# Optimization experiments

Measured on AMD Instinct MI355X. Metric: run time of the kernel, lower is better.

The kernel has to match this reference:

```python
import jax, jax.numpy as jnp
import numpy as np

E, F, NF = 16, 128, 64          # elevators, per-elevator feature size, num_floors
PRE, CI, CH, OUT = 64, 64, 32, 128
R, DROPOFF = 3, 0.333


def _cell(x, h, c, Wih, Whh, bih, bhh, alpha=1.0):
    # torch LSTM cell; alpha scales the candidate-state update (alpha-LSTM).
    g = x @ Wih.T + bih + h @ Whh.T + bhh
    i, f, gg, o = jnp.split(g, 4, axis=-1)
    c2 = jax.nn.sigmoid(f) * c + alpha * jax.nn.sigmoid(i) * jnp.tanh(gg)
    h2 = jax.nn.sigmoid(o) * jnp.tanh(c2)
    return h2, c2


def _forward(features, pre_h, pre_c, out_h, out_c,
             pre_Wih0, pre_Whh0, pre_bih0, pre_bhh0,
             pre_Wih1, pre_Whh1, pre_bih1, pre_bhh1,
             fc_W, fc_b,
             comm_Wih0, comm_Whh0, comm_bih0, comm_bhh0,
             comm_Wih1, comm_Whh1, comm_bih1, comm_bhh1,
             out_Wih, out_Whh, out_bih, out_bhh,
             tar_W, tar_b, dir_W, dir_b):
    # alpha schedule: round r uses dropoff**r, same alpha for all E elevators in a round
    alphas = jnp.repeat(jnp.float32(DROPOFF) ** jnp.arange(R, dtype=jnp.float32), E)

    def step(carry, feat_t):
        ph, pc, oh, oc = carry                       # [E,2,PRE] x2, [E,OUT] x2
        feat = feat_t.reshape(E, F)
        # 2-layer preprocess LSTM, seq len 1, vectorized over elevators
        h0, c0 = _cell(feat, ph[:, 0], pc[:, 0], pre_Wih0, pre_Whh0, pre_bih0, pre_bhh0)
        h1, c1 = _cell(h0,   ph[:, 1], pc[:, 1], pre_Wih1, pre_Whh1, pre_bih1, pre_bhh1)
        x = jax.nn.leaky_relu(h1 @ fc_W.T + fc_b, 0.05)   # [E, CI]
        # sequential communication: rounds x elevators through shared alpha-LSTM state
        xs = jnp.tile(x, (R, 1))                          # [R*E, CI]
        z = jnp.zeros((CH,), feat.dtype)

        def comm_step(cst, xi_a):
            ch0, cc0, ch1, cc1 = cst
            xi, a = xi_a
            nh0, nc0 = _cell(xi, ch0, cc0, comm_Wih0, comm_Whh0, comm_bih0, comm_bhh0, a)
            nh1, nc1 = _cell(nh0, ch1, cc1, comm_Wih1, comm_Whh1, comm_bih1, comm_bhh1, a)
            return (nh0, nc0, nh1, nc1), None

        (ch0, cc0, ch1, cc1), _ = jax.lax.scan(comm_step, (z, z, z, z), (xs, alphas))
        group = jnp.concatenate([cc0, cc1])               # comm cell state flattened [2*CH]
        # postprocessing LSTM (1 layer) + heads, per elevator
        out_in = jnp.concatenate([jnp.broadcast_to(group, (E, 2 * CH)), feat], axis=1)
        noh, noc = _cell(out_in, oh, oc, out_Wih, out_Whh, out_bih, out_bhh)
        tar = jax.nn.softmax(noh @ tar_W.T + tar_b, axis=-1)
        dire = jax.nn.softmax(noh @ dir_W.T + dir_b, axis=-1)
        out = jnp.concatenate([tar, dire], axis=1)        # [E, NF+3]
        new_carry = (jnp.stack([h0, h1], 1), jnp.stack([c0, c1], 1), noh, noc)
        return new_carry, out

    _, outs = jax.lax.scan(step, (pre_h, pre_c, out_h, out_c), features)
    return outs  # [B, E, NF+3]


def setup_inputs() -> dict:
    key = jax.random.key(0)
    ks = iter(jax.random.split(key, 40))

    def p(shape, fan):
        return jax.random.uniform(next(ks), shape, jnp.float32, -1.0, 1.0) / np.sqrt(fan)

    B = 2048
    return {
        "features": jax.random.normal(next(ks), (B, E * F), jnp.float32),
        "pre_h": jnp.zeros((E, 2, PRE), jnp.float32),
        "pre_c": jnp.zeros((E, 2, PRE), jnp.float32),
        "out_h": jnp.zeros((E, OUT), jnp.float32),
        "out_c": jnp.zeros((E, OUT), jnp.float32),
        "pre_Wih0": p((4 * PRE, F), PRE), "pre_Whh0": p((4 * PRE, PRE), PRE),
        "pre_bih0": p((4 * PRE,), PRE), "pre_bhh0": p((4 * PRE,), PRE),
        "pre_Wih1": p((4 * PRE, PRE), PRE), "pre_Whh1": p((4 * PRE, PRE), PRE),
        "pre_bih1": p((4 * PRE,), PRE), "pre_bhh1": p((4 * PRE,), PRE),
        "fc_W": p((CI, PRE), PRE), "fc_b": p((CI,), PRE),
        "comm_Wih0": p((4 * CH, CI), CH), "comm_Whh0": p((4 * CH, CH), CH),
        "comm_bih0": p((4 * CH,), CH), "comm_bhh0": p((4 * CH,), CH),
        "comm_Wih1": p((4 * CH, CH), CH), "comm_Whh1": p((4 * CH, CH), CH),
        "comm_bih1": p((4 * CH,), CH), "comm_bhh1": p((4 * CH,), CH),
        "out_Wih": p((4 * OUT, F + 2 * CH), OUT), "out_Whh": p((4 * OUT, OUT), OUT),
        "out_bih": p((4 * OUT,), OUT), "out_bhh": p((4 * OUT,), OUT),
        "tar_W": p((NF, OUT), OUT), "tar_b": p((NF,), OUT),
        "dir_W": p((3, OUT), OUT), "dir_b": p((3,), OUT),
    }


def reference(features, pre_h, pre_c, out_h, out_c,
              pre_Wih0, pre_Whh0, pre_bih0, pre_bhh0,
              pre_Wih1, pre_Whh1, pre_bih1, pre_bhh1,
              fc_W, fc_b,
              comm_Wih0, comm_Whh0, comm_bih0, comm_bhh0,
              comm_Wih1, comm_Whh1, comm_bih1, comm_bhh1,
              out_Wih, out_Whh, out_bih, out_bhh,
              tar_W, tar_b, dir_W, dir_b):
    return _forward(features, pre_h, pre_c, out_h, out_c,
                    pre_Wih0, pre_Whh0, pre_bih0, pre_bhh0,
                    pre_Wih1, pre_Whh1, pre_bih1, pre_bhh1,
                    fc_W, fc_b,
                    comm_Wih0, comm_Whh0, comm_bih0, comm_bhh0,
                    comm_Wih1, comm_Whh1, comm_bih1, comm_bhh1,
                    out_Wih, out_Whh, out_bih, out_bhh,
                    tar_W, tar_b, dir_W, dir_b)
```

## Files before the change

kernel.cpp:

```cpp
#include <hip/hip_runtime.h>
#include <hip/hip_bf16.h>


#define E_ 16
#define F_ 128

typedef int i4 __attribute__((ext_vector_type(4)));
typedef _Float16 hf;
typedef hf hf2 __attribute__((ext_vector_type(2)));

__device__ __forceinline__ float sigf(float x) { return 1.0f / (1.0f + __expf(-x)); }
__device__ __forceinline__ float tanhf_(float x) {
  float e = __expf(2.0f * x);
  return 1.0f - 2.0f / (e + 1.0f);
}
__device__ __forceinline__ float lane_bcast(float v, int k) {
  return __int_as_float(__builtin_amdgcn_readlane(__float_as_int(v), k));
}
__device__ __forceinline__ float fdot2(int a, int b, float c) {
#if __has_builtin(__builtin_amdgcn_fdot2)
  return __builtin_amdgcn_fdot2(__builtin_bit_cast(hf2, a),
                                __builtin_bit_cast(hf2, b), c, false);
#else
  float d;
  asm("v_dot2_f32_f16 %0, %1, %2, %3" : "=v"(d) : "v"(a), "v"(b), "v"(c));
  return d;
#endif
}

__device__ __forceinline__ float dpp_xor1(float x) {
  return __int_as_float(__builtin_amdgcn_update_dpp(
      __float_as_int(x), __float_as_int(x), 0xB1, 0xF, 0xF, true));
}
__device__ __forceinline__ float dpp_xor2(float x) {
  return __int_as_float(__builtin_amdgcn_update_dpp(
      __float_as_int(x), __float_as_int(x), 0x4E, 0xF, 0xF, true));
}

__global__ void f2h_kernel(const float* __restrict__ src, hf* __restrict__ dst, int n) {
  int i = blockIdx.x * 256 + threadIdx.x;
  if (i < n) dst[i] = (hf)src[i];
}

__global__ __launch_bounds__(256) void gemm_k(
    const float* __restrict__ A, int lda,
    const float* __restrict__ W, int ldw, int co,
    const float* __restrict__ b1, const float* __restrict__ b2,
    float* __restrict__ C, int N, int K) {
  __shared__ float As[64 * 65];
  __shared__ float Ws[128 * 65];
  const int tid = threadIdx.x;
  const int m0 = blockIdx.x * 64;
  const int n0 = blockIdx.y * 128;
  const int rr = tid >> 4;
  const int c4 = (tid & 15) << 2;
  const int tm = tid >> 4;
  const int tn = tid & 15;

  float acc[4][8];
#pragma unroll
  for (int i = 0; i < 4; ++i)
#pragma unroll
    for (int j = 0; j < 8; ++j) acc[i][j] = 0.0f;

  for (int kk = 0; kk < K; kk += 64) {
#pragma unroll
    for (int p = 0; p < 4; ++p) {
      const int r = rr + p * 16;
      const float4 v = *(const float4*)(A + (size_t)(m0 + r) * lda + kk + c4);
      float* dst = &As[r * 65 + c4];
      dst[0] = v.x; dst[1] = v.y; dst[2] = v.z; dst[3] = v.w;
    }
#pragma unroll
    for (int p = 0; p < 8; ++p) {
      const int n = rr + p * 16;
      const float4 v = *(const float4*)(W + (size_t)(n0 + n) * ldw + co + kk + c4);
      float* dst = &Ws[n * 65 + c4];
      dst[0] = v.x; dst[1] = v.y; dst[2] = v.z; dst[3] = v.w;
    }
    __syncthreads();
#pragma unroll 4
    for (int k = 0; k < 64; ++k) {
      float a[4], wv[8];
#pragma unroll
      for (int i = 0; i < 4; ++i) a[i] = As[(tm * 4 + i) * 65 + k];
#pragma unroll
      for (int j = 0; j < 8; ++j) wv[j] = Ws[(tn * 8 + j) * 65 + k];
#pragma unroll
      for (int i = 0; i < 4; ++i)
#pragma unroll
        for (int j = 0; j < 8; ++j) acc[i][j] += a[i] * wv[j];
    }
    __syncthreads();
  }
#pragma unroll
  for (int i = 0; i < 4; ++i) {
    const int m = m0 + tm * 4 + i;
#pragma unroll
    for (int j = 0; j < 8; ++j) {
      const int n = n0 + tn * 8 + j;
      float v = acc[i][j];
      if (b1) v += b1[n];
      if (b2) v += b2[n];
      C[(size_t)m * N + n] = v;
    }
  }
}

__global__ __launch_bounds__(576) void k2_pre(
    const float* __restrict__ pg0, const float* __restrict__ preh,
    const float* __restrict__ prec,
    const hf* __restrict__ hWhh0, const hf* __restrict__ hWih1,
    const hf* __restrict__ hWhh1, const hf* __restrict__ hfcW,
    const float* __restrict__ bih1, const float* __restrict__ bhh1,
    const float* __restrict__ fcb, float* __restrict__ xout, int B) {
  const int e = blockIdx.x, tid = threadIdx.x;
  const int wv = tid >> 6, l = tid & 63;
  const int cls = l & 3;
  __shared__ __align__(16) hf h0s[2][64];
  __shared__ __align__(16) hf h1s[2][64];

  int wa[32], wb[32];
  float bias = 0.f, c = 0.f;
  const float* pgp = nullptr;
  int j = 0;

  if (wv < 4) {
    j = wv * 16 + (l >> 2);
    const int r = cls * 64 + j;
    const i4* p0 = (const i4*)(hWhh0 + r * 64);
#pragma unroll
    for (int i = 0; i < 8; ++i) {
      i4 a = p0[i]; wa[4*i]=a.x; wa[4*i+1]=a.y; wa[4*i+2]=a.z; wa[4*i+3]=a.w;
    }
    pgp = pg0 + (size_t)e * 256 + r;
    if (cls == 1) { c = prec[e * 128 + j]; h0s[1][j] = (hf)preh[e * 128 + j]; }
  } else if (wv < 8) {
    j = (wv - 4) * 16 + (l >> 2);
    const int r = cls * 64 + j;
    const i4* p1 = (const i4*)(hWih1 + r * 64);
    const i4* p2 = (const i4*)(hWhh1 + r * 64);
#pragma unroll
    for (int i = 0; i < 8; ++i) {
      i4 a = p1[i]; wa[4*i]=a.x; wa[4*i+1]=a.y; wa[4*i+2]=a.z; wa[4*i+3]=a.w;
      i4 b = p2[i]; wb[4*i]=b.x; wb[4*i+1]=b.y; wb[4*i+2]=b.z; wb[4*i+3]=b.w;
    }
    bias = bih1[cls * 64 + j] + bhh1[cls * 64 + j];
    if (cls == 1) { c = prec[e * 128 + 64 + j]; h1s[1][j] = (hf)preh[e * 128 + 64 + j]; }
  } else {
    j = l;
    const i4* pf = (const i4*)(hfcW + l * 64);
#pragma unroll
    for (int i = 0; i < 8; ++i) {
      i4 a = pf[i]; wa[4*i]=a.x; wa[4*i+1]=a.y; wa[4*i+2]=a.z; wa[4*i+3]=a.w;
    }
    bias = fcb[l];
  }
  __syncthreads();

  auto doL0 = [&](int nn, float pgv) {
    const i4* hp = (const i4*)h0s[(nn + 1) & 1];
    float a0 = 0.f, a1 = 0.f, a2 = 0.f, a3 = 0.f;
#pragma unroll
    for (int i = 0; i < 8; ++i) {
      i4 h = hp[i];
      a0 = fdot2(wa[4*i],   h.x, a0); a1 = fdot2(wa[4*i+1], h.y, a1);
      a2 = fdot2(wa[4*i+2], h.z, a2); a3 = fdot2(wa[4*i+3], h.w, a3);
    }
    const float pre = (a0 + a1) + (a2 + a3) + pgv;
    const float act = (cls == 2) ? tanhf_(pre) : sigf(pre);
    const float p2 = dpp_xor2(act);
    const float ig = act * p2;
    const float p1 = dpp_xor1(ig);
    if (cls == 1) {
      c = act * c + p1;
      h0s[nn & 1][j] = (hf)(p2 * tanhf_(c));
    }
  };
  auto doL1 = [&](int nn) {
    const i4* hp0 = (const i4*)h0s[(nn + 1) & 1];
    const i4* hp1 = (const i4*)h1s[nn & 1];
    float a0 = 0.f, a1 = 0.f, a2 = 0.f, a3 = 0.f;
#pragma unroll
    for (int i = 0; i < 8; ++i) {
      i4 h = hp0[i];
      a0 = fdot2(wa[4*i],   h.x, a0); a1 = fdot2(wa[4*i+1], h.y, a1);
      a2 = fdot2(wa[4*i+2], h.z, a2); a3 = fdot2(wa[4*i+3], h.w, a3);
    }
#pragma unroll
    for (int i = 0; i < 8; ++i) {
      i4 h = hp1[i];
      a0 = fdot2(wb[4*i],   h.x, a0); a1 = fdot2(wb[4*i+1], h.y, a1);
      a2 = fdot2(wb[4*i+2], h.z, a2); a3 = fdot2(wb[4*i+3], h.w, a3);
    }
    const float pre = (a0 + a1) + (a2 + a3) + bias;
    const float act = (cls == 2) ? tanhf_(pre) : sigf(pre);
    const float p2 = dpp_xor2(act);
    const float ig = act * p2;
    const float p1 = dpp_xor1(ig);
    if (cls == 1) {
      c = act * c + p1;
      h1s[(nn + 1) & 1][j] = (hf)(p2 * tanhf_(c));
    }
  };
  auto doFC = [&](int nn) {
    const i4* hp1 = (const i4*)h1s[nn & 1];
    float a0 = 0.f, a1 = 0.f, a2 = 0.f, a3 = 0.f;
#pragma unroll
    for (int i = 0; i < 8; ++i) {
      i4 h = hp1[i];
      a0 = fdot2(wa[4*i],   h.x, a0); a1 = fdot2(wa[4*i+1], h.y, a1);
      a2 = fdot2(wa[4*i+2], h.z, a2); a3 = fdot2(wa[4*i+3], h.w, a3);
    }
    const float xv = (a0 + a1) + (a2 + a3) + bias;
    xout[((size_t)(nn - 2) * E_ + e) * 64 + l] = (xv > 0.f) ? xv : 0.05f * xv;
  };

  float pgA = 0.f, pgB = 0.f;
  if (wv < 4) { pgA = pgp[0]; if (B > 1) pgB = pgp[4096]; }

  for (int n = 0; n < B + 2; ++n) {
    if (wv < 4) {
      if (n < B) {
        const float pgC = (n + 2 < B) ? pgp[(size_t)(n + 2) * 4096] : 0.f;
        doL0(n, pgA);
        pgA = pgB; pgB = pgC;
      }
    } else if (wv < 8) {
      if (n >= 1 && n <= B) doL1(n);
    } else {
      if (n >= 2) doFC(n);
    }
    __syncthreads();
  }
}

__global__ __launch_bounds__(256) void k3_comm(
    const float* __restrict__ gih0, const float* __restrict__ Whh0,
    const float* __restrict__ Wih1, const float* __restrict__ Whh1,
    const float* __restrict__ bih1, const float* __restrict__ bhh1,
    float* __restrict__ grp, int B) {
  const int w = threadIdx.x >> 6;
  const int l = threadIdx.x & 63;
  const int t = blockIdx.x * 4 + w;

  float wh0a[32], wh0b[32], wi1a[32], wi1b[32], wh1a[32], wh1b[32];
#pragma unroll
  for (int i = 0; i < 32; ++i) {
    wh0a[i] = Whh0[l * 32 + i];         wh0b[i] = Whh0[(l + 64) * 32 + i];
    wi1a[i] = Wih1[l * 32 + i];         wi1b[i] = Wih1[(l + 64) * 32 + i];
    wh1a[i] = Whh1[l * 32 + i];         wh1b[i] = Whh1[(l + 64) * 32 + i];
  }
  const float cb1a = bih1[l] + bhh1[l];
  const float cb1b = bih1[l + 64] + bhh1[l + 64];

  float h0 = 0.0f, c0 = 0.0f, h1 = 0.0f, c1 = 0.0f;
  float al = 1.0f;
  const float* gbase = gih0 + (size_t)t * (E_ * 128);
  for (int r = 0; r < 3; ++r) {
    for (int e = 0; e < E_; ++e) {
      float ga = gbase[e * 128 + l];
      float gb = gbase[e * 128 + l + 64];
#pragma unroll
      for (int k = 0; k < 32; ++k) {
        const float hv = lane_bcast(h0, k);
        ga += wh0a[k] * hv;
        gb += wh0b[k] * hv;
      }
      {
        const float fa = __shfl_xor(ga, 32);
        const float ob = __shfl_xor(gb, 32);
        c0 = sigf(fa) * c0 + al * sigf(ga) * tanhf_(gb);
        h0 = sigf(ob) * tanhf_(c0);
      }
      float ga1 = cb1a, gb1 = cb1b;
#pragma unroll
      for (int k = 0; k < 32; ++k) {
        const float hv = lane_bcast(h0, k);
        ga1 += wi1a[k] * hv;
        gb1 += wi1b[k] * hv;
      }
#pragma unroll
      for (int k = 0; k < 32; ++k) {
        const float hv = lane_bcast(h1, k);
        ga1 += wh1a[k] * hv;
        gb1 += wh1b[k] * hv;
      }
      {
        const float fa = __shfl_xor(ga1, 32);
        const float ob = __shfl_xor(gb1, 32);
        c1 = sigf(fa) * c1 + al * sigf(ga1) * tanhf_(gb1);
        h1 = sigf(ob) * tanhf_(c1);
      }
    }
    al *= 0.333f;
  }
  if (l < 32) {
    grp[(size_t)t * 64 + l] = c0;
    grp[(size_t)t * 64 + 32 + l] = c1;
  }
}

__global__ __launch_bounds__(512) void k4_out(
    const float* __restrict__ pgo, const float* __restrict__ gg,
    const float* __restrict__ outh, const float* __restrict__ outc,
    const hf* __restrict__ hWo, float* __restrict__ noh, int B) {
  const int e = blockIdx.x, tid = threadIdx.x;
  const int wv = tid >> 6, l = tid & 63;
  const int cls = l & 3;
  const int j = wv * 16 + (l >> 2);
  const int r = cls * 128 + j;
  __shared__ __align__(16) hf hs[2][128];

  int w[64];
  {
    const i4* pw = (const i4*)(hWo + (size_t)r * 128);
#pragma unroll
    for (int i = 0; i < 16; ++i) {
      i4 a = pw[i]; w[4*i]=a.x; w[4*i+1]=a.y; w[4*i+2]=a.z; w[4*i+3]=a.w;
    }
  }
  float c = 0.f;
  if (cls == 1) { c = outc[e * 128 + j]; hs[1][j] = (hf)outh[e * 128 + j]; }
  __syncthreads();

  const float* pgoP = pgo + (size_t)e * 512 + r;
  const float* ggP  = gg + r;
  float poA = pgoP[0], gA = ggP[0];
  float poB = 0.f, gB = 0.f;
  if (B > 1) { poB = pgoP[8192]; gB = ggP[512]; }

  for (int n = 0; n < B; ++n) {
    float poC = 0.f, gC = 0.f;
    if (n + 2 < B) { poC = pgoP[(size_t)(n + 2) * 8192]; gC = ggP[(size_t)(n + 2) * 512]; }
    const i4* hp = (const i4*)hs[(n + 1) & 1];
    float a0 = 0.f, a1 = 0.f, a2 = 0.f, a3 = 0.f;
#pragma unroll
    for (int i = 0; i < 16; ++i) {
      i4 h = hp[i];
      a0 = fdot2(w[4*i],   h.x, a0); a1 = fdot2(w[4*i+1], h.y, a1);
      a2 = fdot2(w[4*i+2], h.z, a2); a3 = fdot2(w[4*i+3], h.w, a3);
    }
    const float pre = (a0 + a1) + (a2 + a3) + poA + gA;
    const float act = (cls == 2) ? tanhf_(pre) : sigf(pre);
    const float p2 = dpp_xor2(act);
    const float ig = act * p2;
    const float p1 = dpp_xor1(ig);
    if (cls == 1) {
      c = act * c + p1;
      const float h = p2 * tanhf_(c);
      hs[n & 1][j] = (hf)h;
      noh[((size_t)n * E_ + e) * 128 + j] = h;
    }
    __syncthreads();
    poA = poB; gA = gB; poB = poC; gB = gC;
  }
}

__global__ __launch_bounds__(256) void k5_heads(
    const float* __restrict__ noh, const float* __restrict__ tarW,
    const float* __restrict__ tarb, const float* __restrict__ dirW,
    const float* __restrict__ dirb, float* __restrict__ out) {
  __shared__ float tw[128 * 64];
  __shared__ float tb[64];
  const int tid = threadIdx.x;
  for (int idx = tid; idx < 8192; idx += 256) {
    const int j = idx >> 7, k = idx & 127;
    tw[k * 64 + j] = tarW[idx];
  }
  if (tid < 64) tb[tid] = tarb[tid];
  __syncthreads();
  const int w = tid >> 6, l = tid & 63;
  const float db0 = dirb[0], db1 = dirb[1], db2 = dirb[2];

  for (int p = 0; p < 16; ++p) {
    const int row = blockIdx.x * 64 + p * 4 + w;
    const float na = noh[(size_t)row * 128 + l];
    const float nb = noh[(size_t)row * 128 + 64 + l];
    float acc = tb[l];
#pragma unroll
    for (int k = 0; k < 64; ++k) acc += tw[k * 64 + l] * lane_bcast(na, k);
#pragma unroll
    for (int k = 0; k < 64; ++k) acc += tw[(64 + k) * 64 + l] * lane_bcast(nb, k);
    float m = acc;
#pragma unroll
    for (int s = 32; s; s >>= 1) m = fmaxf(m, __shfl_xor(m, s));
    const float ex = __expf(acc - m);
    float sm = ex;
#pragma unroll
    for (int s = 32; s; s >>= 1) sm += __shfl_xor(sm, s);
    out[(size_t)row * 67 + l] = ex / sm;
    float d0 = dirW[l] * na + dirW[64 + l] * nb;
    float d1 = dirW[128 + l] * na + dirW[192 + l] * nb;
    float d2 = dirW[256 + l] * na + dirW[320 + l] * nb;
#pragma unroll
    for (int s = 32; s; s >>= 1) {
      d0 += __shfl_xor(d0, s);
      d1 += __shfl_xor(d1, s);
      d2 += __shfl_xor(d2, s);
    }
    d0 += db0; d1 += db1; d2 += db2;
    const float dm = fmaxf(d0, fmaxf(d1, d2));
    const float e0 = __expf(d0 - dm), e1 = __expf(d1 - dm), e2 = __expf(d2 - dm);
    const float ds = e0 + e1 + e2;
    if (l < 3) out[(size_t)row * 67 + 64 + l] = (l == 0 ? e0 : (l == 1 ? e1 : e2)) / ds;
  }
}

extern "C" void kernel_launch(void* const* d_in, const int* in_sizes, int n_in,
                              void* d_out, int out_size, void* d_ws, size_t ws_size,
                              hipStream_t stream) {
  const float* features = (const float*)d_in[0];
  const float* pre_h    = (const float*)d_in[1];
  const float* pre_c    = (const float*)d_in[2];
  const float* out_h    = (const float*)d_in[3];
  const float* out_c    = (const float*)d_in[4];
  const float* pre_Wih0 = (const float*)d_in[5];
  const float* pre_Whh0 = (const float*)d_in[6];
  const float* pre_bih0 = (const float*)d_in[7];
  const float* pre_bhh0 = (const float*)d_in[8];
  const float* pre_Wih1 = (const float*)d_in[9];
  const float* pre_Whh1 = (const float*)d_in[10];
  const float* pre_bih1 = (const float*)d_in[11];
  const float* pre_bhh1 = (const float*)d_in[12];
  const float* fc_W     = (const float*)d_in[13];
  const float* fc_b     = (const float*)d_in[14];
  const float* comm_Wih0 = (const float*)d_in[15];
  const float* comm_Whh0 = (const float*)d_in[16];
  const float* comm_bih0 = (const float*)d_in[17];
  const float* comm_bhh0 = (const float*)d_in[18];
  const float* comm_Wih1 = (const float*)d_in[19];
  const float* comm_Whh1 = (const float*)d_in[20];
  const float* comm_bih1 = (const float*)d_in[21];
  const float* comm_bhh1 = (const float*)d_in[22];
  const float* out_Wih  = (const float*)d_in[23];
  const float* out_Whh  = (const float*)d_in[24];
  const float* out_bih  = (const float*)d_in[25];
  const float* out_bhh  = (const float*)d_in[26];
  const float* tar_W    = (const float*)d_in[27];
  const float* tar_b    = (const float*)d_in[28];
  const float* dir_W    = (const float*)d_in[29];
  const float* dir_b    = (const float*)d_in[30];

  const int B = in_sizes[0] / (E_ * F_);
  float* ws = (float*)d_ws;
  float* pg0 = ws;
  float* pgo = pg0 + (size_t)B * E_ * 256;
  float* xbf = pgo + (size_t)B * E_ * 512;
  float* gih = xbf + (size_t)B * E_ * 64;
  float* grp = gih + (size_t)B * E_ * 128;
  float* gg  = grp + (size_t)B * 64;
  float* noh = gg + (size_t)B * 512;
  hf* hWhh0 = (hf*)(noh + (size_t)B * E_ * 128);
  hf* hWih1 = hWhh0 + 256 * 64;
  hf* hWhh1 = hWih1 + 256 * 64;
  hf* hfcW  = hWhh1 + 256 * 64;
  hf* hWo   = hfcW + 64 * 64;
  (void)ws_size; (void)n_in; (void)out_size;

  f2h_kernel<<<(256 * 64 + 255) / 256, 256, 0, stream>>>(pre_Whh0, hWhh0, 256 * 64);
  f2h_kernel<<<(256 * 64 + 255) / 256, 256, 0, stream>>>(pre_Wih1, hWih1, 256 * 64);
  f2h_kernel<<<(256 * 64 + 255) / 256, 256, 0, stream>>>(pre_Whh1, hWhh1, 256 * 64);
  f2h_kernel<<<(64 * 64 + 255) / 256, 256, 0, stream>>>(fc_W, hfcW, 64 * 64);
  f2h_kernel<<<(512 * 128 + 255) / 256, 256, 0, stream>>>(out_Whh, hWo, 512 * 128);

  const int MB = B * E_ / 64;

  gemm_k<<<dim3(MB, 2), 256, 0, stream>>>(features, 128, pre_Wih0, 128, 0,
                                          pre_bih0, pre_bhh0, pg0, 256, 128);
  gemm_k<<<dim3(MB, 4), 256, 0, stream>>>(features, 128, out_Wih, 192, 64,
                                          out_bih, out_bhh, pgo, 512, 128);
  k2_pre<<<E_, 576, 0, stream>>>(pg0, pre_h, pre_c, hWhh0, hWih1, hWhh1, hfcW,
                                 pre_bih1, pre_bhh1, fc_b, xbf, B);
  gemm_k<<<dim3(MB, 1), 256, 0, stream>>>(xbf, 64, comm_Wih0, 64, 0,
                                          comm_bih0, comm_bhh0, gih, 128, 64);
  k3_comm<<<B / 4, 256, 0, stream>>>(gih, comm_Whh0, comm_Wih1, comm_Whh1,
                                     comm_bih1, comm_bhh1, grp, B);
  gemm_k<<<dim3(B / 64, 4), 256, 0, stream>>>(grp, 64, out_Wih, 192, 0,
                                              nullptr, nullptr, gg, 512, 64);
  k4_out<<<E_, 512, 0, stream>>>(pgo, gg, out_h, out_c, hWo, noh, B);
  k5_heads<<<B * E_ / 64, 256, 0, stream>>>(noh, tar_W, tar_b, dir_W, dir_b,
                                            (float*)d_out);
}
```

Before: 3.002 ms.

## Halve waves in recurrent LSTM kernels by giving each lane two hidden units

The sequential pre-LSTM and output-LSTM kernels now assign two hidden units per lane, so k2_pre drops from 9 to 5 waves and k4_out from 8 to 4 waves per block. Each lane keeps twice the weight rows in registers and computes two dot products per step. The aim is to cut the cost of the per-step __syncthreads barrier and the number of waves contending inside the serial time loop. The trade-off is higher register pressure, which may cause spills, and more serial work per lane on the critical path of each step.

```diff
diff --git a/kernel.cpp b/kernel.cpp
--- a/kernel.cpp
+++ b/kernel.cpp
@@ -107,7 +107,7 @@
   }
 }
 
-__global__ __launch_bounds__(576) void k2_pre(
+__global__ __launch_bounds__(320, 1) void k2_pre(
     const float* __restrict__ pg0, const float* __restrict__ preh,
     const float* __restrict__ prec,
     const hf* __restrict__ hWhh0, const hf* __restrict__ hWih1,
@@ -116,91 +116,119 @@
     const float* __restrict__ fcb, float* __restrict__ xout, int B) {
   const int e = blockIdx.x, tid = threadIdx.x;
   const int wv = tid >> 6, l = tid & 63;
-  const int cls = l & 3;
+  const int cls = l & 3, q = l >> 2;
   __shared__ __align__(16) hf h0s[2][64];
   __shared__ __align__(16) hf h1s[2][64];
 
-  int wa[32], wb[32];
-  float bias = 0.f, c = 0.f;
-  const float* pgp = nullptr;
-  int j = 0;
-
-  if (wv < 4) {
-    j = wv * 16 + (l >> 2);
-    const int r = cls * 64 + j;
-    const i4* p0 = (const i4*)(hWhh0 + r * 64);
-#pragma unroll
-    for (int i = 0; i < 8; ++i) {
-      i4 a = p0[i]; wa[4*i]=a.x; wa[4*i+1]=a.y; wa[4*i+2]=a.z; wa[4*i+3]=a.w;
-    }
-    pgp = pg0 + (size_t)e * 256 + r;
-    if (cls == 1) { c = prec[e * 128 + j]; h0s[1][j] = (hf)preh[e * 128 + j]; }
-  } else if (wv < 8) {
-    j = (wv - 4) * 16 + (l >> 2);
-    const int r = cls * 64 + j;
-    const i4* p1 = (const i4*)(hWih1 + r * 64);
-    const i4* p2 = (const i4*)(hWhh1 + r * 64);
-#pragma unroll
-    for (int i = 0; i < 8; ++i) {
-      i4 a = p1[i]; wa[4*i]=a.x; wa[4*i+1]=a.y; wa[4*i+2]=a.z; wa[4*i+3]=a.w;
-      i4 b = p2[i]; wb[4*i]=b.x; wb[4*i+1]=b.y; wb[4*i+2]=b.z; wb[4*i+3]=b.w;
-    }
-    bias = bih1[cls * 64 + j] + bhh1[cls * 64 + j];
-    if (cls == 1) { c = prec[e * 128 + 64 + j]; h1s[1][j] = (hf)preh[e * 128 + 64 + j]; }
+  int wa0[32], wa1[32], wb0[32], wb1[32];
+  float bias0 = 0.f, bias1 = 0.f, c0 = 0.f, c1 = 0.f;
+  const float* pgp0 = nullptr;
+  int e0 = 0;
+
+  if (wv < 2) {
+    e0 = wv * 32 + 2 * q;
+    const int r0 = cls * 64 + e0;
+    const i4* p0 = (const i4*)(hWhh0 + r0 * 64);
+    const i4* p1 = (const i4*)(hWhh0 + (r0 + 1) * 64);
+#pragma unroll
+    for (int i = 0; i < 8; ++i) {
+      i4 a = p0[i]; wa0[4*i]=a.x; wa0[4*i+1]=a.y; wa0[4*i+2]=a.z; wa0[4*i+3]=a.w;
+      i4 b = p1[i]; wa1[4*i]=b.x; wa1[4*i+1]=b.y; wa1[4*i+2]=b.z; wa1[4*i+3]=b.w;
+    }
+    pgp0 = pg0 + (size_t)e * 256 + r0;
+    if (cls == 1) {
+      c0 = prec[e * 128 + e0]; c1 = prec[e * 128 + e0 + 1];
+      hf2 hv; hv.x = (hf)preh[e * 128 + e0]; hv.y = (hf)preh[e * 128 + e0 + 1];
+      *(hf2*)&h0s[1][e0] = hv;
+    }
+  } else if (wv < 4) {
+    e0 = (wv - 2) * 32 + 2 * q;
+    const int r0 = cls * 64 + e0;
+    const i4* pi0 = (const i4*)(hWih1 + r0 * 64);
+    const i4* pi1 = (const i4*)(hWih1 + (r0 + 1) * 64);
+    const i4* ph0 = (const i4*)(hWhh1 + r0 * 64);
+    const i4* ph1 = (const i4*)(hWhh1 + (r0 + 1) * 64);
+#pragma unroll
+    for (int i = 0; i < 8; ++i) {
+      i4 a = pi0[i]; wa0[4*i]=a.x; wa0[4*i+1]=a.y; wa0[4*i+2]=a.z; wa0[4*i+3]=a.w;
+      i4 b = pi1[i]; wa1[4*i]=b.x; wa1[4*i+1]=b.y; wa1[4*i+2]=b.z; wa1[4*i+3]=b.w;
+      i4 c_ = ph0[i]; wb0[4*i]=c_.x; wb0[4*i+1]=c_.y; wb0[4*i+2]=c_.z; wb0[4*i+3]=c_.w;
+      i4 d = ph1[i]; wb1[4*i]=d.x; wb1[4*i+1]=d.y; wb1[4*i+2]=d.z; wb1[4*i+3]=d.w;
+    }
+    bias0 = bih1[r0] + bhh1[r0];
+    bias1 = bih1[r0 + 1] + bhh1[r0 + 1];
+    if (cls == 1) {
+      c0 = prec[e * 128 + 64 + e0]; c1 = prec[e * 128 + 64 + e0 + 1];
+      hf2 hv; hv.x = (hf)preh[e * 128 + 64 + e0]; hv.y = (hf)preh[e * 128 + 64 + e0 + 1];
+      *(hf2*)&h1s[1][e0] = hv;
+    }
   } else {
-    j = l;
     const i4* pf = (const i4*)(hfcW + l * 64);
 #pragma unroll
     for (int i = 0; i < 8; ++i) {
-      i4 a = pf[i]; wa[4*i]=a.x; wa[4*i+1]=a.y; wa[4*i+2]=a.z; wa[4*i+3]=a.w;
-    }
-    bias = fcb[l];
+      i4 a = pf[i]; wa0[4*i]=a.x; wa0[4*i+1]=a.y; wa0[4*i+2]=a.z; wa0[4*i+3]=a.w;
+    }
+    bias0 = fcb[l];
   }
   __syncthreads();
 
-  auto doL0 = [&](int nn, float pgv) {
+  auto doL0 = [&](int nn, float pg0v, float pg1v) {
     const i4* hp = (const i4*)h0s[(nn + 1) & 1];
-    float a0 = 0.f, a1 = 0.f, a2 = 0.f, a3 = 0.f;
+    float a0 = 0.f, a1 = 0.f, b0 = 0.f, b1 = 0.f;
 #pragma unroll
     for (int i = 0; i < 8; ++i) {
       i4 h = hp[i];
-      a0 = fdot2(wa[4*i],   h.x, a0); a1 = fdot2(wa[4*i+1], h.y, a1);
-      a2 = fdot2(wa[4*i+2], h.z, a2); a3 = fdot2(wa[4*i+3], h.w, a3);
-    }
-    const float pre = (a0 + a1) + (a2 + a3) + pgv;
-    const float act = (cls == 2) ? tanhf_(pre) : sigf(pre);
-    const float p2 = dpp_xor2(act);
-    const float ig = act * p2;
-    const float p1 = dpp_xor1(ig);
+      a0 = fdot2(wa0[4*i],   h.x, a0); a1 = fdot2(wa0[4*i+1], h.y, a1);
+      a0 = fdot2(wa0[4*i+2], h.z, a0); a1 = fdot2(wa0[4*i+3], h.w, a1);
+      b0 = fdot2(wa1[4*i],   h.x, b0); b1 = fdot2(wa1[4*i+1], h.y, b1);
+      b0 = fdot2(wa1[4*i+2], h.z, b0); b1 = fdot2(wa1[4*i+3], h.w, b1);
+    }
+    const float pre0 = a0 + a1 + pg0v;
+    const float pre1 = b0 + b1 + pg1v;
+    const float act0 = (cls == 2) ? tanhf_(pre0) : sigf(pre0);
+    const float act1 = (cls == 2) ? tanhf_(pre1) : sigf(pre1);
+    const float p20 = dpp_xor2(act0), p21 = dpp_xor2(act1);
+    const float ig0 = act0 * p20, ig1 = act1 * p21;
+    const float p10 = dpp_xor1(ig0), p11 = dpp_xor1(ig1);
     if (cls == 1) {
-      c = act * c + p1;
-      h0s[nn & 1][j] = (hf)(p2 * tanhf_(c));
+      c0 = act0 * c0 + p10;
+      c1 = act1 * c1 + p11;
+      hf2 hv; hv.x = (hf)(p20 * tanhf_(c0)); hv.y = (hf)(p21 * tanhf_(c1));
+      *(hf2*)&h0s[nn & 1][e0] = hv;
     }
   };
   auto doL1 = [&](int nn) {
     const i4* hp0 = (const i4*)h0s[(nn + 1) & 1];
     const i4* hp1 = (const i4*)h1s[nn & 1];
-    float a0 = 0.f, a1 = 0.f, a2 = 0.f, a3 = 0.f;
+    float a0 = 0.f, a1 = 0.f, b0 = 0.f, b1 = 0.f;
 #pragma unroll
     for (int i = 0; i < 8; ++i) {
       i4 h = hp0[i];
-      a0 = fdot2(wa[4*i],   h.x, a0); a1 = fdot2(wa[4*i+1], h.y, a1);
-      a2 = fdot2(wa[4*i+2], h.z, a2); a3 = fdot2(wa[4*i+3], h.w, a3);
+      a0 = fdot2(wa0[4*i],   h.x, a0); a1 = fdot2(wa0[4*i+1], h.y, a1);
+      a0 = fdot2(wa0[4*i+2], h.z, a0); a1 = fdot2(wa0[4*i+3], h.w, a1);
+      b0 = fdot2(wa1[4*i],   h.x, b0); b1 = fdot2(wa1[4*i+1], h.y, b1);
+      b0 = fdot2(wa1[4*i+2], h.z, b0); b1 = fdot2(wa1[4*i+3], h.w, b1);
     }
 #pragma unroll
     for (int i = 0; i < 8; ++i) {
       i4 h = hp1[i];
-      a0 = fdot2(wb[4*i],   h.x, a0); a1 = fdot2(wb[4*i+1], h.y, a1);
-      a2 = fdot2(wb[4*i+2], h.z, a2); a3 = fdot2(wb[4*i+3], h.w, a3);
-    }
-    const float pre = (a0 + a1) + (a2 + a3) + bias;
-    const float act = (cls == 2) ? tanhf_(pre) : sigf(pre);
-    const float p2 = dpp_xor2(act);
-    const float ig = act * p2;
-    const float p1 = dpp_xor1(ig);
+      a0 = fdot2(wb0[4*i],   h.x, a0); a1 = fdot2(wb0[4*i+1], h.y, a1);
+      a0 = fdot2(wb0[4*i+2], h.z, a0); a1 = fdot2(wb0[4*i+3], h.w, a1);
+      b0 = fdot2(wb1[4*i],   h.x, b0); b1 = fdot2(wb1[4*i+1], h.y, b1);
+      b0 = fdot2(wb1[4*i+2], h.z, b0); b1 = fdot2(wb1[4*i+3], h.w, b1);
+    }
+    const float pre0 = a0 + a1 + bias0;
+    const float pre1 = b0 + b1 + bias1;
+    const float act0 = (cls == 2) ? tanhf_(pre0) : sigf(pre0);
+    const float act1 = (cls == 2) ? tanhf_(pre1) : sigf(pre1);
+    const float p20 = dpp_xor2(act0), p21 = dpp_xor2(act1);
+    const float ig0 = act0 * p20, ig1 = act1 * p21;
+    const float p10 = dpp_xor1(ig0), p11 = dpp_xor1(ig1);
     if (cls == 1) {
-      c = act * c + p1;
-      h1s[(nn + 1) & 1][j] = (hf)(p2 * tanhf_(c));
+      c0 = act0 * c0 + p10;
+      c1 = act1 * c1 + p11;
+      hf2 hv; hv.x = (hf)(p20 * tanhf_(c0)); hv.y = (hf)(p21 * tanhf_(c1));
+      *(hf2*)&h1s[(nn + 1) & 1][e0] = hv;
     }
   };
   auto doFC = [&](int nn) {
@@ -209,24 +237,29 @@
 #pragma unroll
     for (int i = 0; i < 8; ++i) {
       i4 h = hp1[i];
-      a0 = fdot2(wa[4*i],   h.x, a0); a1 = fdot2(wa[4*i+1], h.y, a1);
-      a2 = fdot2(wa[4*i+2], h.z, a2); a3 = fdot2(wa[4*i+3], h.w, a3);
-    }
-    const float xv = (a0 + a1) + (a2 + a3) + bias;
+      a0 = fdot2(wa0[4*i],   h.x, a0); a1 = fdot2(wa0[4*i+1], h.y, a1);
+      a2 = fdot2(wa0[4*i+2], h.z, a2); a3 = fdot2(wa0[4*i+3], h.w, a3);
+    }
+    const float xv = (a0 + a1) + (a2 + a3) + bias0;
     xout[((size_t)(nn - 2) * E_ + e) * 64 + l] = (xv > 0.f) ? xv : 0.05f * xv;
   };
 
-  float pgA = 0.f, pgB = 0.f;
-  if (wv < 4) { pgA = pgp[0]; if (B > 1) pgB = pgp[4096]; }
+  float pgA0 = 0.f, pgA1 = 0.f, pgB0 = 0.f, pgB1 = 0.f;
+  if (wv < 2) {
+    pgA0 = pgp0[0]; pgA1 = pgp0[1];
+    if (B > 1) { pgB0 = pgp0[4096]; pgB1 = pgp0[4097]; }
+  }
 
   for (int n = 0; n < B + 2; ++n) {
-    if (wv < 4) {
+    if (wv < 2) {
       if (n < B) {
-        const float pgC = (n + 2 < B) ? pgp[(size_t)(n + 2) * 4096] : 0.f;
-        doL0(n, pgA);
-        pgA = pgB; pgB = pgC;
+        float pgC0 = 0.f, pgC1 = 0.f;
+        if (n + 2 < B) { pgC0 = pgp0[(size_t)(n + 2) * 4096];
+                         pgC1 = pgp0[(size_t)(n + 2) * 4096 + 1]; }
+        doL0(n, pgA0, pgA1);
+        pgA0 = pgB0; pgA1 = pgB1; pgB0 = pgC0; pgB1 = pgC1;
       }
-    } else if (wv < 8) {
+    } else if (wv < 4) {
       if (n >= 1 && n <= B) doL1(n);
     } else {
       if (n >= 2) doFC(n);
@@ -301,59 +334,83 @@
   }
 }
 
-__global__ __launch_bounds__(512) void k4_out(
+__global__ __launch_bounds__(256, 1) void k4_out(
     const float* __restrict__ pgo, const float* __restrict__ gg,
     const float* __restrict__ outh, const float* __restrict__ outc,
     const hf* __restrict__ hWo, float* __restrict__ noh, int B) {
   const int e = blockIdx.x, tid = threadIdx.x;
   const int wv = tid >> 6, l = tid & 63;
-  const int cls = l & 3;
-  const int j = wv * 16 + (l >> 2);
-  const int r = cls * 128 + j;
+  const int cls = l & 3, q = l >> 2;
+  const int e0 = wv * 32 + 2 * q;
+  const int r0 = cls * 128 + e0;
   __shared__ __align__(16) hf hs[2][128];
 
-  int w[64];
+  int w0_[64], w1_[64];
   {
-    const i4* pw = (const i4*)(hWo + (size_t)r * 128);
+    const i4* p0 = (const i4*)(hWo + (size_t)r0 * 128);
+    const i4* p1 = (const i4*)(hWo + (size_t)(r0 + 1) * 128);
 #pragma unroll
     for (int i = 0; i < 16; ++i) {
-      i4 a = pw[i]; w[4*i]=a.x; w[4*i+1]=a.y; w[4*i+2]=a.z; w[4*i+3]=a.w;
-    }
-  }
-  float c = 0.f;
-  if (cls == 1) { c = outc[e * 128 + j]; hs[1][j] = (hf)outh[e * 128 + j]; }
+      i4 a = p0[i]; w0_[4*i]=a.x; w0_[4*i+1]=a.y; w0_[4*i+2]=a.z; w0_[4*i+3]=a.w;
+      i4 b = p1[i]; w1_[4*i]=b.x; w1_[4*i+1]=b.y; w1_[4*i+2]=b.z; w1_[4*i+3]=b.w;
+    }
+  }
+  float c0 = 0.f, c1 = 0.f;
+  if (cls == 1) {
+    c0 = outc[e * 128 + e0]; c1 = outc[e * 128 + e0 + 1];
+    hf2 hv; hv.x = (hf)outh[e * 128 + e0]; hv.y = (hf)outh[e * 128 + e0 + 1];
+    *(hf2*)&hs[1][e0] = hv;
+  }
   __syncthreads();
 
-  const float* pgoP = pgo + (size_t)e * 512 + r;
-  const float* ggP  = gg + r;
-  float poA = pgoP[0], gA = ggP[0];
-  float poB = 0.f, gB = 0.f;
-  if (B > 1) { poB = pgoP[8192]; gB = ggP[512]; }
-
-  for (int n = 0; n < B; ++n) {
-    float poC = 0.f, gC = 0.f;
-    if (n + 2 < B) { poC = pgoP[(size_t)(n + 2) * 8192]; gC = ggP[(size_t)(n + 2) * 512]; }
-    const i4* hp = (const i4*)hs[(n + 1) & 1];
-    float a0 = 0.f, a1 = 0.f, a2 = 0.f, a3 = 0.f;
+  const float* pgoP = pgo + (size_t)e * 512 + r0;
+  const float* ggP  = gg + r0;
+
+  auto doStep = [&](int nn, float po0, float po1, float g0, float g1) {
+    const i4* hp = (const i4*)hs[(nn + 1) & 1];
+    float a0 = 0.f, a1 = 0.f, b0 = 0.f, b1 = 0.f;
 #pragma unroll
     for (int i = 0; i < 16; ++i) {
       i4 h = hp[i];
-      a0 = fdot2(w[4*i],   h.x, a0); a1 = fdot2(w[4*i+1], h.y, a1);
-      a2 = fdot2(w[4*i+2], h.z, a2); a3 = fdot2(w[4*i+3], h.w, a3);
-    }
-    const float pre = (a0 + a1) + (a2 + a3) + poA + gA;
-    const float act = (cls == 2) ? tanhf_(pre) : sigf(pre);
-    const float p2 = dpp_xor2(act);
-    const float ig = act * p2;
-    const float p1 = dpp_xor1(ig);
+      a0 = fdot2(w0_[4*i],   h.x, a0); a1 = fdot2(w0_[4*i+1], h.y, a1);
+      a0 = fdot2(w0_[4*i+2], h.z, a0); a1 = fdot2(w0_[4*i+3], h.w, a1);
+      b0 = fdot2(w1_[4*i],   h.x, b0); b1 = fdot2(w1_[4*i+1], h.y, b1);
+      b0 = fdot2(w1_[4*i+2], h.z, b0); b1 = fdot2(w1_[4*i+3], h.w, b1);
+    }
+    const float pre0 = a0 + a1 + po0 + g0;
+    const float pre1 = b0 + b1 + po1 + g1;
+    const float act0 = (cls == 2) ? tanhf_(pre0) : sigf(pre0);
+    const float act1 = (cls == 2) ? tanhf_(pre1) : sigf(pre1);
+    const float p20 = dpp_xor2(act0), p21 = dpp_xor2(act1);
+    const float ig0 = act0 * p20, ig1 = act1 * p21;
+    const float p10 = dpp_xor1(ig0), p11 = dpp_xor1(ig1);
     if (cls == 1) {
-      c = act * c + p1;
-      const float h = p2 * tanhf_(c);
-      hs[n & 1][j] = (hf)h;
-      noh[((size_t)n * E_ + e) * 128 + j] = h;
-    }
+      c0 = act0 * c0 + p10;
+      c1 = act1 * c1 + p11;
+      const float h0v = p20 * tanhf_(c0);
+      const float h1v = p21 * tanhf_(c1);
+      hf2 hv; hv.x = (hf)h0v; hv.y = (hf)h1v;
+      *(hf2*)&hs[nn & 1][e0] = hv;
+      float2 nv; nv.x = h0v; nv.y = h1v;
+      *(float2*)&noh[((size_t)nn * E_ + e) * 128 + e0] = nv;
+    }
+  };
+
+  float oA0 = pgoP[0], oA1 = pgoP[1];
+  float gA0 = ggP[0], gA1 = ggP[1];
+  float oB0 = 0.f, oB1 = 0.f, gB0 = 0.f, gB1 = 0.f;
+  if (B > 1) { oB0 = pgoP[8192]; oB1 = pgoP[8193]; gB0 = ggP[512]; gB1 = ggP[513]; }
+
+  for (int n = 0; n < B; ++n) {
+    float oC0 = 0.f, oC1 = 0.f, gC0 = 0.f, gC1 = 0.f;
+    if (n + 2 < B) {
+      oC0 = pgoP[(size_t)(n + 2) * 8192]; oC1 = pgoP[(size_t)(n + 2) * 8192 + 1];
+      gC0 = ggP[(size_t)(n + 2) * 512];   gC1 = ggP[(size_t)(n + 2) * 512 + 1];
+    }
+    doStep(n, oA0, oA1, gA0, gA1);
     __syncthreads();
-    poA = poB; gA = gB; poB = poC; gB = gC;
+    oA0 = oB0; oA1 = oB1; gA0 = gB0; gA1 = gB1;
+    oB0 = oC0; oB1 = oC1; gB0 = gC0; gB1 = gC1;
   }
 }
 
@@ -470,7 +527,7 @@
                                           pre_bih0, pre_bhh0, pg0, 256, 128);
   gemm_k<<<dim3(MB, 4), 256, 0, stream>>>(features, 128, out_Wih, 192, 64,
                                           out_bih, out_bhh, pgo, 512, 128);
-  k2_pre<<<E_, 576, 0, stream>>>(pg0, pre_h, pre_c, hWhh0, hWih1, hWhh1, hfcW,
+  k2_pre<<<E_, 320, 0, stream>>>(pg0, pre_h, pre_c, hWhh0, hWih1, hWhh1, hfcW,
                                  pre_bih1, pre_bhh1, fc_b, xbf, B);
   gemm_k<<<dim3(MB, 1), 256, 0, stream>>>(xbf, 64, comm_Wih0, 64, 0,
                                           comm_bih0, comm_bhh0, gih, 128, 64);
@@ -478,7 +535,7 @@
                                      comm_bih1, comm_bhh1, grp, B);
   gemm_k<<<dim3(B / 64, 4), 256, 0, stream>>>(grp, 64, out_Wih, 192, 0,
                                               nullptr, nullptr, gg, 512, 64);
-  k4_out<<<E_, 512, 0, stream>>>(pgo, gg, out_h, out_c, hWo, noh, B);
+  k4_out<<<E_, 256, 0, stream>>>(pgo, gg, out_h, out_c, hWo, noh, B);
   k5_heads<<<B * E_ / 64, 256, 0, stream>>>(noh, tar_W, tar_b, dir_W, dir_b,
                                             (float*)d_out);
 }
```

Measured after the change: 3.336 ms. 11.1% more time.

## Prefetch per-step gate inputs into LDS ring buffers via dedicated producer wave

Applied to the files above, without the earlier changes.

In the sequential recurrent kernels k2_pre and k4_out, per-timestep precomputed gate inputs are now staged into 16-slot shared-memory ring buffers eight steps ahead. A spare wave does the loads (in k4_out an added ninth wave also drains the output h to global memory), so compute waves no longer wait on global loads or issue global stores on the serial critical path. This adds LDS footprint, an extra wave, and more shared-memory traffic per step.

```diff
diff --git a/kernel.cpp b/kernel.cpp
--- a/kernel.cpp
+++ b/kernel.cpp
@@ -119,25 +119,24 @@
   const int cls = l & 3;
   __shared__ __align__(16) hf h0s[2][64];
   __shared__ __align__(16) hf h1s[2][64];
+  __shared__ float pgr[16][256];
 
   int wa[32], wb[32];
   float bias = 0.f, c = 0.f;
-  const float* pgp = nullptr;
-  int j = 0;
+  int j = 0, r = 0;
 
   if (wv < 4) {
     j = wv * 16 + (l >> 2);
-    const int r = cls * 64 + j;
+    r = cls * 64 + j;
     const i4* p0 = (const i4*)(hWhh0 + r * 64);
 #pragma unroll
     for (int i = 0; i < 8; ++i) {
       i4 a = p0[i]; wa[4*i]=a.x; wa[4*i+1]=a.y; wa[4*i+2]=a.z; wa[4*i+3]=a.w;
     }
-    pgp = pg0 + (size_t)e * 256 + r;
     if (cls == 1) { c = prec[e * 128 + j]; h0s[1][j] = (hf)preh[e * 128 + j]; }
   } else if (wv < 8) {
     j = (wv - 4) * 16 + (l >> 2);
-    const int r = cls * 64 + j;
+    r = cls * 64 + j;
     const i4* p1 = (const i4*)(hWih1 + r * 64);
     const i4* p2 = (const i4*)(hWhh1 + r * 64);
 #pragma unroll
@@ -145,7 +144,7 @@
       i4 a = p1[i]; wa[4*i]=a.x; wa[4*i+1]=a.y; wa[4*i+2]=a.z; wa[4*i+3]=a.w;
       i4 b = p2[i]; wb[4*i]=b.x; wb[4*i+1]=b.y; wb[4*i+2]=b.z; wb[4*i+3]=b.w;
     }
-    bias = bih1[cls * 64 + j] + bhh1[cls * 64 + j];
+    bias = bih1[r] + bhh1[r];
     if (cls == 1) { c = prec[e * 128 + 64 + j]; h1s[1][j] = (hf)preh[e * 128 + 64 + j]; }
   } else {
     j = l;
@@ -156,9 +155,14 @@
     }
     bias = fcb[l];
   }
+  for (int idx = tid; idx < 8 * 256; idx += 576) {
+    const int t = idx >> 8, rr_ = idx & 255;
+    pgr[t][rr_] = (t < B) ? pg0[(size_t)e * 256 + (size_t)t * 4096 + rr_] : 0.f;
+  }
   __syncthreads();
 
-  auto doL0 = [&](int nn, float pgv) {
+  auto doL0 = [&](int nn) {
+    const float pgv = pgr[nn & 15][r];
     const i4* hp = (const i4*)h0s[(nn + 1) & 1];
     float a0 = 0.f, a1 = 0.f, a2 = 0.f, a3 = 0.f;
 #pragma unroll
@@ -216,20 +220,20 @@
     xout[((size_t)(nn - 2) * E_ + e) * 64 + l] = (xv > 0.f) ? xv : 0.05f * xv;
   };
 
-  float pgA = 0.f, pgB = 0.f;
-  if (wv < 4) { pgA = pgp[0]; if (B > 1) pgB = pgp[4096]; }
-
   for (int n = 0; n < B + 2; ++n) {
     if (wv < 4) {
-      if (n < B) {
-        const float pgC = (n + 2 < B) ? pgp[(size_t)(n + 2) * 4096] : 0.f;
-        doL0(n, pgA);
-        pgA = pgB; pgB = pgC;
-      }
+      if (n < B) doL0(n);
     } else if (wv < 8) {
       if (n >= 1 && n <= B) doL1(n);
     } else {
       if (n >= 2) doFC(n);
+      const int t = n + 8;
+      if (t < B) {
+        const float* src = pg0 + (size_t)e * 256 + (size_t)t * 4096;
+        float v0 = src[l], v1 = src[64 + l], v2 = src[128 + l], v3 = src[192 + l];
+        float* dst = pgr[t & 15];
+        dst[l] = v0; dst[64 + l] = v1; dst[128 + l] = v2; dst[192 + l] = v3;
+      }
     }
     __syncthreads();
   }
@@ -301,19 +305,22 @@
   }
 }
 
-__global__ __launch_bounds__(512) void k4_out(
+__global__ __launch_bounds__(576) void k4_out(
     const float* __restrict__ pgo, const float* __restrict__ gg,
     const float* __restrict__ outh, const float* __restrict__ outc,
     const hf* __restrict__ hWo, float* __restrict__ noh, int B) {
   const int e = blockIdx.x, tid = threadIdx.x;
   const int wv = tid >> 6, l = tid & 63;
   const int cls = l & 3;
-  const int j = wv * 16 + (l >> 2);
+  const int j = (wv < 8) ? (wv * 16 + (l >> 2)) : 0;
   const int r = cls * 128 + j;
   __shared__ __align__(16) hf hs[2][128];
+  __shared__ float pgor[16][512];
+  __shared__ float ggr[16][512];
+  __shared__ float nohr[16][128];
 
   int w[64];
-  {
+  if (wv < 8) {
     const i4* pw = (const i4*)(hWo + (size_t)r * 128);
 #pragma unroll
     for (int i = 0; i < 16; ++i) {
@@ -321,19 +328,18 @@
     }
   }
   float c = 0.f;
-  if (cls == 1) { c = outc[e * 128 + j]; hs[1][j] = (hf)outh[e * 128 + j]; }
+  if (wv < 8 && cls == 1) { c = outc[e * 128 + j]; hs[1][j] = (hf)outh[e * 128 + j]; }
+  for (int idx = tid; idx < 8 * 512; idx += 576) {
+    const int t = idx >> 9, rr_ = idx & 511;
+    pgor[t][rr_] = (t < B) ? pgo[(size_t)e * 512 + (size_t)t * 8192 + rr_] : 0.f;
+    ggr[t][rr_]  = (t < B) ? gg[(size_t)t * 512 + rr_] : 0.f;
+  }
   __syncthreads();
 
-  const float* pgoP = pgo + (size_t)e * 512 + r;
-  const float* ggP  = gg + r;
-  float poA = pgoP[0], gA = ggP[0];
-  float poB = 0.f, gB = 0.f;
-  if (B > 1) { poB = pgoP[8192]; gB = ggP[512]; }
-
-  for (int n = 0; n < B; ++n) {
-    float poC = 0.f, gC = 0.f;
-    if (n + 2 < B) { poC = pgoP[(size_t)(n + 2) * 8192]; gC = ggP[(size_t)(n + 2) * 512]; }
-    const i4* hp = (const i4*)hs[(n + 1) & 1];
+  auto doStep = [&](int nn) {
+    const float po = pgor[nn & 15][r];
+    const float gv = ggr[nn & 15][r];
+    const i4* hp = (const i4*)hs[(nn + 1) & 1];
     float a0 = 0.f, a1 = 0.f, a2 = 0.f, a3 = 0.f;
 #pragma unroll
     for (int i = 0; i < 16; ++i) {
@@ -341,7 +347,7 @@
       a0 = fdot2(w[4*i],   h.x, a0); a1 = fdot2(w[4*i+1], h.y, a1);
       a2 = fdot2(w[4*i+2], h.z, a2); a3 = fdot2(w[4*i+3], h.w, a3);
     }
-    const float pre = (a0 + a1) + (a2 + a3) + poA + gA;
+    const float pre = (a0 + a1) + (a2 + a3) + po + gv;
     const float act = (cls == 2) ? tanhf_(pre) : sigf(pre);
     const float p2 = dpp_xor2(act);
     const float ig = act * p2;
@@ -349,11 +355,46 @@
     if (cls == 1) {
       c = act * c + p1;
       const float h = p2 * tanhf_(c);
-      hs[n & 1][j] = (hf)h;
-      noh[((size_t)n * E_ + e) * 128 + j] = h;
+      hs[nn & 1][j] = (hf)h;
+      nohr[nn & 15][j] = h;
+    }
+  };
+
+  for (int n = 0; n < B; ++n) {
+    if (wv < 8) {
+      doStep(n);
+    } else {
+      if (n >= 8) {
+        const int m = n - 8;
+        const float v0 = nohr[m & 15][l];
+        const float v1 = nohr[m & 15][64 + l];
+        noh[((size_t)m * E_ + e) * 128 + l] = v0;
+        noh[((size_t)m * E_ + e) * 128 + 64 + l] = v1;
+      }
+      const int t = n + 8;
+      if (t < B) {
+        const float* ps = pgo + (size_t)e * 512 + (size_t)t * 8192;
+        const float* gs = gg + (size_t)t * 512;
+        float tp[8], tg[8];
+#pragma unroll
+        for (int i = 0; i < 8; ++i) tp[i] = ps[i * 64 + l];
+#pragma unroll
+        for (int i = 0; i < 8; ++i) tg[i] = gs[i * 64 + l];
+        float* pd = pgor[t & 15];
+        float* gd = ggr[t & 15];
+#pragma unroll
+        for (int i = 0; i < 8; ++i) pd[i * 64 + l] = tp[i];
+#pragma unroll
+        for (int i = 0; i < 8; ++i) gd[i * 64 + l] = tg[i];
+      }
     }
     __syncthreads();
-    poA = poB; gA = gB; poB = poC; gB = gC;
+  }
+  if (wv == 8) {
+    for (int m = (B >= 8 ? B - 8 : 0); m < B; ++m) {
+      noh[((size_t)m * E_ + e) * 128 + l] = nohr[m & 15][l];
+      noh[((size_t)m * E_ + e) * 128 + 64 + l] = nohr[m & 15][64 + l];
+    }
   }
 }
 
@@ -478,7 +519,7 @@
                                      comm_bih1, comm_bhh1, grp, B);
   gemm_k<<<dim3(B / 64, 4), 256, 0, stream>>>(grp, 64, out_Wih, 192, 0,
                                               nullptr, nullptr, gg, 512, 64);
-  k4_out<<<E_, 512, 0, stream>>>(pgo, gg, out_h, out_c, hWo, noh, B);
+  k4_out<<<E_, 576, 0, stream>>>(pgo, gg, out_h, out_c, hWo, noh, B);
   k5_heads<<<B * E_ / 64, 256, 0, stream>>>(noh, tar_W, tar_b, dir_W, dir_b,
                                             (float*)d_out);
 }
```

Result: slower. 3.727 ms (+24.2%).
